# Kernel tuning notes

Measured on AMD Instinct MI355X. Metric: run time of the kernel, lower is better.

## Reference

```python
import jax, jax.numpy as jnp
import numpy as np

N_SENT = 20  # sentence_number


def setup_inputs() -> dict:
    key = jax.random.key(0)
    k1, k2, k3, k4, k5 = jax.random.split(key, 5)
    B, S, D, U = 2048, 800, 100, 50
    inputs = jax.random.normal(k1, (B, S + 1, D), dtype=jnp.float32)
    # keras 'random_normal' initializer default stddev = 0.05
    vw = 0.05 * jax.random.normal(k2, (U, 1), dtype=jnp.float32)
    wh = 0.05 * jax.random.normal(k3, (U, D), dtype=jnp.float32)
    wu = 0.05 * jax.random.normal(k4, (U, D), dtype=jnp.float32)
    bw = 0.05 * jax.random.normal(k5, (U, 1), dtype=jnp.float32)
    return {"inputs": inputs, "vw": vw, "wh": wh, "wu": wu, "bw": bw}


def reference(inputs, vw, wh, wu, bw):
    # inputs: [B, S+1, D]; last row of each item is the user vector
    sent = inputs[:, :-1, :]          # [B, S, D]
    uvec = inputs[:, -1, :]           # [B, D]
    B, S, D = sent.shape
    sec = S // N_SENT
    h = sent.reshape(B, N_SENT, sec, D)               # sections of sentences
    # wu @ user_vec + bw  -> per-batch additive bias  [B, units]
    wub = uvec @ wu.T + bw[:, 0]
    # tanh(h @ wh.T + wub)                              [B, n, s, units]
    t = jnp.tanh(jnp.einsum('bnsd,ud->bnsu', h, wh) + wub[:, None, None, :])
    e = jnp.einsum('bnsu,u->bns', t, vw[:, 0])          # attention logits
    alpha = jax.nn.softmax(e, axis=-1)                  # softmax over section
    out = jnp.einsum('bns,bnsd->bnd', alpha, h)         # weighted pooling
    return out  # [B, N_SENT, D]
```

## Files before the change

### kernel.cpp

```cpp
#include <hip/hip_runtime.h>
#include <hip/hip_bf16.h>
#include <stdint.h>

#define NB    2048
#define NSENT 20
#define SEC   40
#define DD    100
#define UU    50
#define SP1   801
#define STRIDE 136

typedef __attribute__((ext_vector_type(8))) short bf16x8;
typedef __attribute__((ext_vector_type(4))) float f32x4;

__device__ __forceinline__ unsigned f2bf(float f) {
  unsigned u = __float_as_uint(f);
  unsigned r = u + 0x7fffu + ((u >> 16) & 1u);
  return r >> 16;
}

__global__ __launch_bounds__(256, 4) void doc_kernel(
    const float* __restrict__ inputs, const float* __restrict__ vw,
    const float* __restrict__ wh, const float* __restrict__ wu,
    const float* __restrict__ bw, float* __restrict__ out) {
  __shared__ __align__(16) unsigned short hs[2][48 * STRIDE];
  __shared__ __align__(16) float epart[3 * 16 * 4];
  __shared__ float alphas[SEC];
  __shared__ __align__(16) float2 opart[50 * 4];

  const int tid  = threadIdx.x;
  const int w    = tid >> 6, lane = tid & 63;
  const int col  = lane & 15, grp = lane >> 4;
  const int b    = blockIdx.x;

  const float4* base4 = (const float4*)(inputs + (size_t)b * SP1 * DD);

  float4 stage[4];
  #pragma unroll
  for (int j = 0; j < 4; ++j) {
    int idx = j * 256 + tid;
    if (idx < 1000) stage[j] = base4[idx];
  }

  {
    uint4 z; z.x = z.y = z.z = z.w = 0u;
    uint4* p = (uint4*)&hs[0][0];
    #pragma unroll 1
    for (int i = tid; i < 2 * 48 * STRIDE / 8; i += 256) p[i] = z;
  }

  bf16x8 afrag[4];
  {
    int u = w * 16 + col;
    #pragma unroll
    for (int kt = 0; kt < 4; ++kt) {
      bf16x8 f;
      #pragma unroll
      for (int j = 0; j < 8; ++j) {
        int k = kt * 32 + grp * 8 + j;
        float v = (u < UU && k < DD) ? wh[u * DD + k] : 0.f;
        f[j] = (short)f2bf(v);
      }
      afrag[kt] = f;
    }
  }

  float wubacc;
  {
    int ur = lane < UU ? lane : UU - 1;
    const float4* uv4 = (const float4*)(inputs + ((size_t)b * SP1 + SP1 - 1) * DD);
    const float4* wr4 = (const float4*)(wu + ur * DD);
    float a0 = bw[ur];
    #pragma unroll 5
    for (int q = 0; q < 25; ++q) {
      float4 uq = uv4[q], wq = wr4[q];
      a0 = fmaf(uq.x, wq.x, a0); a0 = fmaf(uq.y, wq.y, a0);
      a0 = fmaf(uq.z, wq.z, a0); a0 = fmaf(uq.w, wq.w, a0);
    }
    wubacc = a0;
  }
  float vwr[4], wubr[4];
  #pragma unroll
  for (int r = 0; r < 4; ++r) {
    int u = w * 16 + grp * 4 + r;
    float wv = __shfl(wubacc, u & 63);
    bool val = (u < UU);
    vwr[r]  = val ? vw[u] : 0.f;
    wubr[r] = val ? wv : 0.f;
  }

  __syncthreads();

  float* outb = out + (size_t)b * NSENT * DD;
  int cur = 0;

  #pragma unroll 1
  for (int t = 0; t < NSENT; ++t) {
    #pragma unroll
    for (int j = 0; j < 4; ++j) {
      int idx = j * 256 + tid;
      if (idx < 1000) {
        int row = idx / 25, c4 = idx - row * 25;
        uint2 wv;
        wv.x = f2bf(stage[j].x) | (f2bf(stage[j].y) << 16);
        wv.y = f2bf(stage[j].z) | (f2bf(stage[j].w) << 16);
        *(uint2*)&hs[cur][row * STRIDE + c4 * 4] = wv;
      }
    }
    __syncthreads();

    if (t + 1 < NSENT) {
      const float4* nb4 = base4 + (size_t)(t + 1) * 1000;
      #pragma unroll
      for (int j = 0; j < 4; ++j) {
        int idx = j * 256 + tid;
        if (idx < 1000) stage[j] = nb4[idx];
      }
    }
    __builtin_amdgcn_sched_barrier(0);

    f32x4 acc[3];
    #pragma unroll
    for (int st = 0; st < 3; ++st) { f32x4 z = {0.f,0.f,0.f,0.f}; acc[st] = z; }
    #pragma unroll
    for (int kt = 0; kt < 4; ++kt) {
      #pragma unroll
      for (int st = 0; st < 3; ++st) {
        bf16x8 hf = *(const bf16x8*)&hs[cur][(st * 16 + col) * STRIDE + kt * 32 + grp * 8];
        acc[st] = __builtin_amdgcn_mfma_f32_16x16x32_bf16(afrag[kt], hf, acc[st], 0, 0, 0);
      }
    }

    #pragma unroll
    for (int st = 0; st < 3; ++st) {
      float s = 0.f;
      #pragma unroll
      for (int r = 0; r < 4; ++r) {
        float x = acc[st][r] + wubr[r];
        x = fminf(fmaxf(x, -15.f), 15.f);
        float E = __expf(2.f * x);
        float tt = 1.f - 2.f * __builtin_amdgcn_rcpf(E + 1.f);
        s = fmaf(tt, vwr[r], s);
      }
      s += __shfl_xor(s, 16);
      s += __shfl_xor(s, 32);
      if (grp == 0) epart[st * 64 + col * 4 + w] = s;
    }
    __syncthreads();

    f32x4 q0 = *(const f32x4*)&epart[0 * 64 + col * 4];
    f32x4 q1 = *(const f32x4*)&epart[1 * 64 + col * 4];
    f32x4 q2 = *(const f32x4*)&epart[2 * 64 + col * 4];
    float e0 = (q0[0] + q0[1]) + (q0[2] + q0[3]);
    float e1 = (q1[0] + q1[1]) + (q1[2] + q1[3]);
    float e2 = (q2[0] + q2[1]) + (q2[2] + q2[3]);
    float mx = fmaxf(e0, e1);
    if (col < 8) mx = fmaxf(mx, e2);
    mx = fmaxf(mx, __shfl_xor(mx, 1));
    mx = fmaxf(mx, __shfl_xor(mx, 2));
    mx = fmaxf(mx, __shfl_xor(mx, 4));
    mx = fmaxf(mx, __shfl_xor(mx, 8));
    float p0 = __expf(e0 - mx);
    float p1 = __expf(e1 - mx);
    float p2 = (col < 8) ? __expf(e2 - mx) : 0.f;
    float sum = p0 + p1 + p2;
    sum += __shfl_xor(sum, 1);
    sum += __shfl_xor(sum, 2);
    sum += __shfl_xor(sum, 4);
    sum += __shfl_xor(sum, 8);
    float rinv = __builtin_amdgcn_rcpf(sum);
    if (w == 0 && grp == 0) {
      alphas[col]      = p0 * rinv;
      alphas[16 + col] = p1 * rinv;
      if (col < 8) alphas[32 + col] = p2 * rinv;
    }
    __syncthreads();

    if (lane < 50) {
      float f0 = 0.f, f1 = 0.f;
      #pragma unroll
      for (int i = 0; i < 10; ++i) {
        int s = w * 10 + i;
        float a = alphas[s];
        unsigned hh = *(const unsigned*)&hs[cur][s * STRIDE + lane * 2];
        f0 = fmaf(a, __uint_as_float(hh << 16), f0);
        f1 = fmaf(a, __uint_as_float(hh & 0xffff0000u), f1);
      }
      float2 o; o.x = f0; o.y = f1;
      opart[lane * 4 + w] = o;
    }
    __syncthreads();

    if (w == 0 && lane < 50) {
      f32x4 a0 = *(const f32x4*)&opart[lane * 4];
      f32x4 a1 = *(const f32x4*)&opart[lane * 4 + 2];
      float2 o;
      o.x = (a0[0] + a0[2]) + (a1[0] + a1[2]);
      o.y = (a0[1] + a0[3]) + (a1[1] + a1[3]);
      *(float2*)(outb + t * DD + lane * 2) = o;
    }
    cur ^= 1;
  }
}

extern "C" void kernel_launch(void* const* d_in, const int* in_sizes, int n_in,
                              void* d_out, int out_size, void* d_ws, size_t ws_size,
                              hipStream_t stream) {
  const float* inputs = (const float*)d_in[0];
  const float* vw     = (const float*)d_in[1];
  const float* wh     = (const float*)d_in[2];
  const float* wu     = (const float*)d_in[3];
  const float* bw     = (const float*)d_in[4];
  float* out = (float*)d_out;

  doc_kernel<<<NB, 256, 0, stream>>>(inputs, vw, wh, wu, bw, out);
}
```

Measured before the change: 165.4 us.

## Stream fp32 sections into LDS via global_load_lds and convert to bf16 at fragment load

Replaces the register staging and bf16 repacking into LDS with direct global-to-LDS asynchronous loads of fp32 section data, double-buffered. The data is converted to bf16 only when building MFMA fragments, and the weighted pooling now reads fp32 directly from LDS with each wave producing 25 output columns, which removes the partial-sum reduction stage. It also drops the tanh input clamp and the softmax max subtraction, which saves instructions but risks overflow for large logits. LDS use roughly doubles per buffer, which may reduce occupancy, and the async prefetch relies on the later barriers for completion.

Result: slower. 184.0 us (+11.3%).

```diff
diff --git a/kernel.cpp b/kernel.cpp
--- a/kernel.cpp
+++ b/kernel.cpp
@@ -8,7 +8,7 @@
 #define DD    100
 #define UU    50
 #define SP1   801
-#define STRIDE 136
+#define FBE   4832
 
 typedef __attribute__((ext_vector_type(8))) short bf16x8;
 typedef __attribute__((ext_vector_type(4))) float f32x4;
@@ -19,34 +19,44 @@
   return r >> 16;
 }
 
+__device__ __forceinline__ bf16x8 cvt8(f32x4 a, f32x4 b) {
+  union { unsigned u[4]; bf16x8 v; } r;
+  asm("v_cvt_pk_bf16_f32 %0, %1, %2" : "=v"(r.u[0]) : "v"(a[0]), "v"(a[1]));
+  asm("v_cvt_pk_bf16_f32 %0, %1, %2" : "=v"(r.u[1]) : "v"(a[2]), "v"(a[3]));
+  asm("v_cvt_pk_bf16_f32 %0, %1, %2" : "=v"(r.u[2]) : "v"(b[0]), "v"(b[1]));
+  asm("v_cvt_pk_bf16_f32 %0, %1, %2" : "=v"(r.u[3]) : "v"(b[2]), "v"(b[3]));
+  return r.v;
+}
+
+#define GL16(gp, lp) __builtin_amdgcn_global_load_lds( \
+    (const __attribute__((address_space(1))) unsigned*)(const void*)(gp), \
+    (__attribute__((address_space(3))) unsigned*)(void*)(lp), 16, 0, 0)
+
 __global__ __launch_bounds__(256, 4) void doc_kernel(
     const float* __restrict__ inputs, const float* __restrict__ vw,
     const float* __restrict__ wh, const float* __restrict__ wu,
     const float* __restrict__ bw, float* __restrict__ out) {
-  __shared__ __align__(16) unsigned short hs[2][48 * STRIDE];
+  __shared__ __align__(16) float fbuf[2][FBE];
   __shared__ __align__(16) float epart[3 * 16 * 4];
   __shared__ float alphas[SEC];
-  __shared__ __align__(16) float2 opart[50 * 4];
 
   const int tid  = threadIdx.x;
   const int w    = tid >> 6, lane = tid & 63;
   const int col  = lane & 15, grp = lane >> 4;
   const int b    = blockIdx.x;
 
-  const float4* base4 = (const float4*)(inputs + (size_t)b * SP1 * DD);
-
-  float4 stage[4];
+  const float* base = inputs + (size_t)b * SP1 * DD;
+
   #pragma unroll
-  for (int j = 0; j < 4; ++j) {
-    int idx = j * 256 + tid;
-    if (idx < 1000) stage[j] = base4[idx];
-  }
-
-  {
-    uint4 z; z.x = z.y = z.z = z.w = 0u;
-    uint4* p = (uint4*)&hs[0][0];
-    #pragma unroll 1
-    for (int i = tid; i < 2 * 48 * STRIDE / 8; i += 256) p[i] = z;
+  for (int c = 0; c < 4; ++c) {
+    int chunk = 4 * w + c;
+    int g = chunk * 64 + lane;
+    if (g < 1000) GL16(base + g * 4, &fbuf[0][chunk * 256]);
+  }
+
+  for (int i = tid; i < 2 * (FBE - 4000); i += 256) {
+    int bb = i >= (FBE - 4000);
+    fbuf[bb][4000 + (i - bb * (FBE - 4000))] = 0.f;
   }
 
   bf16x8 afrag[4];
@@ -96,29 +106,18 @@
 
   #pragma unroll 1
   for (int t = 0; t < NSENT; ++t) {
-    #pragma unroll
-    for (int j = 0; j < 4; ++j) {
-      int idx = j * 256 + tid;
-      if (idx < 1000) {
-        int row = idx / 25, c4 = idx - row * 25;
-        uint2 wv;
-        wv.x = f2bf(stage[j].x) | (f2bf(stage[j].y) << 16);
-        wv.y = f2bf(stage[j].z) | (f2bf(stage[j].w) << 16);
-        *(uint2*)&hs[cur][row * STRIDE + c4 * 4] = wv;
-      }
-    }
-    __syncthreads();
-
     if (t + 1 < NSENT) {
-      const float4* nb4 = base4 + (size_t)(t + 1) * 1000;
-      #pragma unroll
-      for (int j = 0; j < 4; ++j) {
-        int idx = j * 256 + tid;
-        if (idx < 1000) stage[j] = nb4[idx];
-      }
-    }
-    __builtin_amdgcn_sched_barrier(0);
-
+      const float* nb = base + (size_t)(t + 1) * (SEC * DD);
+      float* lb = &fbuf[cur ^ 1][0];
+      #pragma unroll
+      for (int c = 0; c < 4; ++c) {
+        int chunk = 4 * w + c;
+        int g = chunk * 64 + lane;
+        if (g < 1000) GL16(nb + g * 4, lb + chunk * 256);
+      }
+    }
+
+    const float* fb = &fbuf[cur][0];
     f32x4 acc[3];
     #pragma unroll
     for (int st = 0; st < 3; ++st) { f32x4 z = {0.f,0.f,0.f,0.f}; acc[st] = z; }
@@ -126,7 +125,10 @@
     for (int kt = 0; kt < 4; ++kt) {
       #pragma unroll
       for (int st = 0; st < 3; ++st) {
-        bf16x8 hf = *(const bf16x8*)&hs[cur][(st * 16 + col) * STRIDE + kt * 32 + grp * 8];
+        int off = (st * 16 + col) * DD + kt * 32 + grp * 8;
+        f32x4 fa = *(const f32x4*)(fb + off);
+        f32x4 fbv = *(const f32x4*)(fb + off + 4);
+        bf16x8 hf = cvt8(fa, fbv);
         acc[st] = __builtin_amdgcn_mfma_f32_16x16x32_bf16(afrag[kt], hf, acc[st], 0, 0, 0);
       }
     }
@@ -137,7 +139,6 @@
       #pragma unroll
       for (int r = 0; r < 4; ++r) {
         float x = acc[st][r] + wubr[r];
-        x = fminf(fmaxf(x, -15.f), 15.f);
         float E = __expf(2.f * x);
         float tt = 1.f - 2.f * __builtin_amdgcn_rcpf(E + 1.f);
         s = fmaf(tt, vwr[r], s);
@@ -148,21 +149,15 @@
     }
     __syncthreads();
 
-    f32x4 q0 = *(const f32x4*)&epart[0 * 64 + col * 4];
-    f32x4 q1 = *(const f32x4*)&epart[1 * 64 + col * 4];
-    f32x4 q2 = *(const f32x4*)&epart[2 * 64 + col * 4];
+    f32x4 q0 = *(const f32x4*)&epart[col * 4];
+    f32x4 q1 = *(const f32x4*)&epart[64 + col * 4];
+    f32x4 q2 = *(const f32x4*)&epart[128 + col * 4];
     float e0 = (q0[0] + q0[1]) + (q0[2] + q0[3]);
     float e1 = (q1[0] + q1[1]) + (q1[2] + q1[3]);
     float e2 = (q2[0] + q2[1]) + (q2[2] + q2[3]);
-    float mx = fmaxf(e0, e1);
-    if (col < 8) mx = fmaxf(mx, e2);
-    mx = fmaxf(mx, __shfl_xor(mx, 1));
-    mx = fmaxf(mx, __shfl_xor(mx, 2));
-    mx = fmaxf(mx, __shfl_xor(mx, 4));
-    mx = fmaxf(mx, __shfl_xor(mx, 8));
-    float p0 = __expf(e0 - mx);
-    float p1 = __expf(e1 - mx);
-    float p2 = (col < 8) ? __expf(e2 - mx) : 0.f;
+    float p0 = __expf(e0);
+    float p1 = __expf(e1);
+    float p2 = (col < 8) ? __expf(e2) : 0.f;
     float sum = p0 + p1 + p2;
     sum += __shfl_xor(sum, 1);
     sum += __shfl_xor(sum, 2);
@@ -176,29 +171,17 @@
     }
     __syncthreads();
 
-    if (lane < 50) {
-      float f0 = 0.f, f1 = 0.f;
-      #pragma unroll
-      for (int i = 0; i < 10; ++i) {
-        int s = w * 10 + i;
-        float a = alphas[s];
-        unsigned hh = *(const unsigned*)&hs[cur][s * STRIDE + lane * 2];
-        f0 = fmaf(a, __uint_as_float(hh << 16), f0);
-        f1 = fmaf(a, __uint_as_float(hh & 0xffff0000u), f1);
-      }
-      float2 o; o.x = f0; o.y = f1;
-      opart[lane * 4 + w] = o;
+    if (lane < 25) {
+      const float* colp = fb + 25 * w + lane;
+      float a0 = 0.f, a1 = 0.f;
+      #pragma unroll
+      for (int s = 0; s < SEC; s += 2) {
+        a0 = fmaf(alphas[s],     colp[s * DD], a0);
+        a1 = fmaf(alphas[s + 1], colp[(s + 1) * DD], a1);
+      }
+      outb[t * DD + 25 * w + lane] = a0 + a1;
     }
     __syncthreads();
-
-    if (w == 0 && lane < 50) {
-      f32x4 a0 = *(const f32x4*)&opart[lane * 4];
-      f32x4 a1 = *(const f32x4*)&opart[lane * 4 + 2];
-      float2 o;
-      o.x = (a0[0] + a0[2]) + (a1[0] + a1[2]);
-      o.y = (a0[1] + a0[3]) + (a1[1] + a1[3]);
-      *(float2*)(outb + t * DD + lane * 2) = o;
-    }
     cur ^= 1;
   }
 }
```

## Switch to 32x32x16 MFMA with bias folded into GEMM and swizzled LDS

Applied to the files above, without the earlier changes.

Replaces the 16x16x32 MFMA tiling with 32x32x16 MFMAs split across warps by unit-half and sentence-half. The per-batch bias is folded into the GEMM as an extra K column (a constant 1.0 in the h tile and wub in the weights). The LDS layout is XOR-swizzled to cut bank conflicts, and conversion uses hardware packed bf16 converts. The softmax drops max-subtraction and the alpha LDS round-trip and sync in favour of shuffles. Risks: the bias is now rounded to bf16, and softmax without max subtraction could overflow for large logits.

After: 257.0 us. 55.4% more time.

```diff
diff --git a/kernel.cpp b/kernel.cpp
--- a/kernel.cpp
+++ b/kernel.cpp
@@ -8,30 +8,40 @@
 #define DD    100
 #define UU    50
 #define SP1   801
-#define STRIDE 136
-
-typedef __attribute__((ext_vector_type(8))) short bf16x8;
-typedef __attribute__((ext_vector_type(4))) float f32x4;
+#define ROWB  272
+#define HBUFB (64 * ROWB)
+
+typedef short bf16x8 __attribute__((ext_vector_type(8)));
+typedef short bf16x4 __attribute__((ext_vector_type(4)));
+typedef float f32x16 __attribute__((ext_vector_type(16)));
 
 __device__ __forceinline__ unsigned f2bf(float f) {
   unsigned u = __float_as_uint(f);
-  unsigned r = u + 0x7fffu + ((u >> 16) & 1u);
-  return r >> 16;
-}
+  return (u + 0x7fffu + ((u >> 16) & 1u)) >> 16;
+}
+
+__device__ __forceinline__ void cvt8(float4 a, float4 b, unsigned* o) {
+  asm("v_cvt_pk_bf16_f32 %0, %1, %2" : "=v"(o[0]) : "v"(a.x), "v"(a.y));
+  asm("v_cvt_pk_bf16_f32 %0, %1, %2" : "=v"(o[1]) : "v"(a.z), "v"(a.w));
+  asm("v_cvt_pk_bf16_f32 %0, %1, %2" : "=v"(o[2]) : "v"(b.x), "v"(b.y));
+  asm("v_cvt_pk_bf16_f32 %0, %1, %2" : "=v"(o[3]) : "v"(b.z), "v"(b.w));
+}
+
+#define KEY(row) ((((row) >> 3) & 3) << 3)
 
 __global__ __launch_bounds__(256, 4) void doc_kernel(
     const float* __restrict__ inputs, const float* __restrict__ vw,
     const float* __restrict__ wh, const float* __restrict__ wu,
     const float* __restrict__ bw, float* __restrict__ out) {
-  __shared__ __align__(16) unsigned short hs[2][48 * STRIDE];
-  __shared__ __align__(16) float epart[3 * 16 * 4];
-  __shared__ float alphas[SEC];
-  __shared__ __align__(16) float2 opart[50 * 4];
-
-  const int tid  = threadIdx.x;
-  const int w    = tid >> 6, lane = tid & 63;
-  const int col  = lane & 15, grp = lane >> 4;
-  const int b    = blockIdx.x;
+  __shared__ __align__(16) unsigned char hsb[2 * HBUFB];
+  __shared__ __align__(16) float epartf[64 * 2];
+  __shared__ __align__(16) float opartf[50 * 10];
+
+  const int tid = threadIdx.x;
+  const int w = tid >> 6, lane = tid & 63;
+  const int ut = w & 1, st = w >> 1;
+  const int l31 = lane & 31, hh = lane >> 5;
+  const int b = blockIdx.x;
 
   const float4* base4 = (const float4*)(inputs + (size_t)b * SP1 * DD);
 
@@ -44,67 +54,86 @@
 
   {
     uint4 z; z.x = z.y = z.z = z.w = 0u;
-    uint4* p = (uint4*)&hs[0][0];
+    uint4* p = (uint4*)hsb;
     #pragma unroll 1
-    for (int i = tid; i < 2 * 48 * STRIDE / 8; i += 256) p[i] = z;
-  }
-
-  bf16x8 afrag[4];
-  {
-    int u = w * 16 + col;
-    #pragma unroll
-    for (int kt = 0; kt < 4; ++kt) {
-      bf16x8 f;
-      #pragma unroll
-      for (int j = 0; j < 8; ++j) {
-        int k = kt * 32 + grp * 8 + j;
-        float v = (u < UU && k < DD) ? wh[u * DD + k] : 0.f;
-        f[j] = (short)f2bf(v);
-      }
-      afrag[kt] = f;
-    }
-  }
-
-  float wubacc;
-  {
-    int ur = lane < UU ? lane : UU - 1;
+    for (int i = tid; i < 2 * HBUFB / 16; i += 256) p[i] = z;
+  }
+
+  int cvta[4];
+  #pragma unroll
+  for (int j = 0; j < 4; ++j) {
+    int idx = j * 256 + tid;
+    int row = idx / 25, c4 = idx - row * 25;
+    cvta[j] = (row * ROWB + c4 * 8) ^ KEY(row);
+  }
+
+  const int u = l31 + 32 * ut;
+  float wubv = 0.f;
+  if (u < UU) {
     const float4* uv4 = (const float4*)(inputs + ((size_t)b * SP1 + SP1 - 1) * DD);
-    const float4* wr4 = (const float4*)(wu + ur * DD);
-    float a0 = bw[ur];
+    const float4* wr4 = (const float4*)(wu + u * DD);
+    float a0 = bw[u];
     #pragma unroll 5
     for (int q = 0; q < 25; ++q) {
       float4 uq = uv4[q], wq = wr4[q];
       a0 = fmaf(uq.x, wq.x, a0); a0 = fmaf(uq.y, wq.y, a0);
       a0 = fmaf(uq.z, wq.z, a0); a0 = fmaf(uq.w, wq.w, a0);
     }
-    wubacc = a0;
-  }
-  float vwr[4], wubr[4];
-  #pragma unroll
-  for (int r = 0; r < 4; ++r) {
-    int u = w * 16 + grp * 4 + r;
-    float wv = __shfl(wubacc, u & 63);
-    bool val = (u < UU);
-    vwr[r]  = val ? vw[u] : 0.f;
-    wubr[r] = val ? wv : 0.f;
-  }
-
+    wubv = a0;
+  }
+
+  bf16x8 afrag[8];
+  #pragma unroll
+  for (int kt = 0; kt < 8; ++kt) {
+    int k0 = 16 * kt + 8 * hh;
+    float4 fa = {0.f,0.f,0.f,0.f}, fb = {0.f,0.f,0.f,0.f};
+    if (u < UU) {
+      if (k0 + 3 <= 99) fa = *(const float4*)(wh + u * DD + k0);
+      if (k0 + 7 <= 99) fb = *(const float4*)(wh + u * DD + k0 + 4);
+    }
+    union { unsigned uu[4]; bf16x8 v; } r;
+    cvt8(fa, fb, r.uu);
+    if (kt == 6 && hh == 0 && u < UU) {
+      union { unsigned short s[8]; bf16x8 v; } t2; t2.v = r.v;
+      t2.s[4] = (unsigned short)f2bf(wubv);
+      r.v = t2.v;
+    }
+    afrag[kt] = r.v;
+  }
+
+  float vwr[16];
+  #pragma unroll
+  for (int i = 0; i < 16; ++i) {
+    int row = (i & 3) + 8 * (i >> 2) + 4 * hh;
+    int ui = 32 * ut + row;
+    vwr[i] = (ui < UU) ? vw[ui] : 0.f;
+  }
+
+  if (tid < 80) {
+    int buf = tid / SEC, s = tid - buf * SEC;
+    int byte = buf * HBUFB + ((s * ROWB + 200) ^ KEY(s));
+    *(unsigned short*)(hsb + byte) = 0x3F80;
+  }
   __syncthreads();
 
+  const int brow = l31 + 32 * st;
+  const int brb = brow * ROWB, bkey = KEY(brow);
+
   float* outb = out + (size_t)b * NSENT * DD;
-  int cur = 0;
 
   #pragma unroll 1
   for (int t = 0; t < NSENT; ++t) {
+    unsigned char* hcur = hsb + (t & 1) * HBUFB;
+
     #pragma unroll
     for (int j = 0; j < 4; ++j) {
       int idx = j * 256 + tid;
       if (idx < 1000) {
-        int row = idx / 25, c4 = idx - row * 25;
-        uint2 wv;
-        wv.x = f2bf(stage[j].x) | (f2bf(stage[j].y) << 16);
-        wv.y = f2bf(stage[j].z) | (f2bf(stage[j].w) << 16);
-        *(uint2*)&hs[cur][row * STRIDE + c4 * 4] = wv;
+        unsigned o[4];
+        cvt8(make_float4(stage[j].x, stage[j].y, stage[j].z, stage[j].w),
+             make_float4(0.f,0.f,0.f,0.f), o);
+        uint2 wv; wv.x = o[0]; wv.y = o[1];
+        *(uint2*)(hcur + cvta[j]) = wv;
       }
     }
     __syncthreads();
@@ -119,87 +148,62 @@
     }
     __builtin_amdgcn_sched_barrier(0);
 
-    f32x4 acc[3];
+    f32x16 acc = {0.f,0.f,0.f,0.f,0.f,0.f,0.f,0.f,0.f,0.f,0.f,0.f,0.f,0.f,0.f,0.f};
     #pragma unroll
-    for (int st = 0; st < 3; ++st) { f32x4 z = {0.f,0.f,0.f,0.f}; acc[st] = z; }
+    for (int kt = 0; kt < 8; ++kt) {
+      int x = 32 * kt + 16 * hh;
+      bf16x4 lo = *(const bf16x4*)(hcur + ((brb + x) ^ bkey));
+      bf16x4 hi = *(const bf16x4*)(hcur + ((brb + x + 8) ^ bkey));
+      bf16x8 bf = __builtin_shufflevector(lo, hi, 0,1,2,3,4,5,6,7);
+      acc = __builtin_amdgcn_mfma_f32_32x32x16_bf16(afrag[kt], bf, acc, 0, 0, 0);
+    }
+
+    float ep = 0.f;
     #pragma unroll
-    for (int kt = 0; kt < 4; ++kt) {
-      #pragma unroll
-      for (int st = 0; st < 3; ++st) {
-        bf16x8 hf = *(const bf16x8*)&hs[cur][(st * 16 + col) * STRIDE + kt * 32 + grp * 8];
-        acc[st] = __builtin_amdgcn_mfma_f32_16x16x32_bf16(afrag[kt], hf, acc[st], 0, 0, 0);
-      }
-    }
-
-    #pragma unroll
-    for (int st = 0; st < 3; ++st) {
-      float s = 0.f;
-      #pragma unroll
-      for (int r = 0; r < 4; ++r) {
-        float x = acc[st][r] + wubr[r];
-        x = fminf(fmaxf(x, -15.f), 15.f);
-        float E = __expf(2.f * x);
-        float tt = 1.f - 2.f * __builtin_amdgcn_rcpf(E + 1.f);
-        s = fmaf(tt, vwr[r], s);
-      }
-      s += __shfl_xor(s, 16);
-      s += __shfl_xor(s, 32);
-      if (grp == 0) epart[st * 64 + col * 4 + w] = s;
-    }
+    for (int i = 0; i < 16; ++i) {
+      float E = exp2f(acc[i] * 2.885390081777927f);
+      float tt = 1.f - 2.f * __builtin_amdgcn_rcpf(E + 1.f);
+      ep = fmaf(tt, vwr[i], ep);
+    }
+    ep += __shfl_xor(ep, 32);
+    if (lane < 32)
+      epartf[(32 * st + l31) * 2 + ut] = ep;
     __syncthreads();
 
-    f32x4 q0 = *(const f32x4*)&epart[0 * 64 + col * 4];
-    f32x4 q1 = *(const f32x4*)&epart[1 * 64 + col * 4];
-    f32x4 q2 = *(const f32x4*)&epart[2 * 64 + col * 4];
-    float e0 = (q0[0] + q0[1]) + (q0[2] + q0[3]);
-    float e1 = (q1[0] + q1[1]) + (q1[2] + q1[3]);
-    float e2 = (q2[0] + q2[1]) + (q2[2] + q2[3]);
-    float mx = fmaxf(e0, e1);
-    if (col < 8) mx = fmaxf(mx, e2);
-    mx = fmaxf(mx, __shfl_xor(mx, 1));
-    mx = fmaxf(mx, __shfl_xor(mx, 2));
-    mx = fmaxf(mx, __shfl_xor(mx, 4));
-    mx = fmaxf(mx, __shfl_xor(mx, 8));
-    float p0 = __expf(e0 - mx);
-    float p1 = __expf(e1 - mx);
-    float p2 = (col < 8) ? __expf(e2 - mx) : 0.f;
-    float sum = p0 + p1 + p2;
+    float2 e2 = (lane < SEC) ? *(const float2*)&epartf[2 * lane]
+                             : make_float2(0.f, 0.f);
+    float p = (lane < SEC) ? __expf(e2.x + e2.y) : 0.f;
+    float sum = p;
     sum += __shfl_xor(sum, 1);
     sum += __shfl_xor(sum, 2);
     sum += __shfl_xor(sum, 4);
     sum += __shfl_xor(sum, 8);
-    float rinv = __builtin_amdgcn_rcpf(sum);
-    if (w == 0 && grp == 0) {
-      alphas[col]      = p0 * rinv;
-      alphas[16 + col] = p1 * rinv;
-      if (col < 8) alphas[32 + col] = p2 * rinv;
-    }
-    __syncthreads();
+    sum += __shfl_xor(sum, 16);
+    sum += __shfl_xor(sum, 32);
+    float pr = p * __builtin_amdgcn_rcpf(sum);
 
     if (lane < 50) {
       float f0 = 0.f, f1 = 0.f;
       #pragma unroll
       for (int i = 0; i < 10; ++i) {
-        int s = w * 10 + i;
-        float a = alphas[s];
-        unsigned hh = *(const unsigned*)&hs[cur][s * STRIDE + lane * 2];
-        f0 = fmaf(a, __uint_as_float(hh << 16), f0);
-        f1 = fmaf(a, __uint_as_float(hh & 0xffff0000u), f1);
+        int s = 10 * w + i;
+        float a = __shfl(pr, s);
+        unsigned hv = *(const unsigned*)(hcur + ((s * ROWB + 4 * lane) ^ KEY(s)));
+        f0 = fmaf(a, __uint_as_float(hv << 16), f0);
+        f1 = fmaf(a, __uint_as_float(hv & 0xffff0000u), f1);
       }
-      float2 o; o.x = f0; o.y = f1;
-      opart[lane * 4 + w] = o;
+      *(float2*)&opartf[lane * 10 + w * 2] = make_float2(f0, f1);
     }
     __syncthreads();
 
     if (w == 0 && lane < 50) {
-      f32x4 a0 = *(const f32x4*)&opart[lane * 4];
-      f32x4 a1 = *(const f32x4*)&opart[lane * 4 + 2];
+      const float2* op = (const float2*)&opartf[lane * 10];
+      float2 o0 = op[0], o1 = op[1], o2 = op[2], o3 = op[3];
       float2 o;
-      o.x = (a0[0] + a0[2]) + (a1[0] + a1[2]);
-      o.y = (a0[1] + a0[3]) + (a1[1] + a1[3]);
-      *(float2*)(outb + t * DD + lane * 2) = o;
-    }
-    cur ^= 1;
+      o.x = (o0.x + o1.x) + (o2.x + o3.x);
+      o.y = (o0.y + o1.y) + (o2.y + o3.y);
+      *(float2*)(outb + t * DD + 2 * lane) = o;
+    }
   }
 }
 
```

## Compute softmax per wave and pool over all sentences to drop block barriers

Applied to the files above, without the earlier changes.

Every wave now computes the 40-way softmax redundantly in its own lanes. It broadcasts the alpha weights with readlane, and each wave pools 25 output dims across all sentences, writing straight to global memory. This removes the alphas and opart shared buffers and two __syncthreads per iteration. It also drops the max-subtraction in the softmax and the tanh input clamp, which is safe only while the logits stay bounded by the vw magnitudes. Smaller changes: bf16 conversion uses the v_cvt_pk_bf16_f32 instruction, store offsets are precomputed, and the launch-bounds occupancy hint rises from 4 to 5.

Result: slower. 171.8 us (+3.9%).

```diff
diff --git a/kernel.cpp b/kernel.cpp
--- a/kernel.cpp
+++ b/kernel.cpp
@@ -10,23 +10,20 @@
 #define SP1   801
 #define STRIDE 136
 
-typedef __attribute__((ext_vector_type(8))) short bf16x8;
-typedef __attribute__((ext_vector_type(4))) float f32x4;
+typedef short bf16x8 __attribute__((ext_vector_type(8)));
+typedef float f32x4 __attribute__((ext_vector_type(4)));
 
 __device__ __forceinline__ unsigned f2bf(float f) {
   unsigned u = __float_as_uint(f);
-  unsigned r = u + 0x7fffu + ((u >> 16) & 1u);
-  return r >> 16;
+  return (u + 0x7fffu + ((u >> 16) & 1u)) >> 16;
 }
 
-__global__ __launch_bounds__(256, 4) void doc_kernel(
+__global__ __launch_bounds__(256, 5) void doc_kernel(
     const float* __restrict__ inputs, const float* __restrict__ vw,
     const float* __restrict__ wh, const float* __restrict__ wu,
     const float* __restrict__ bw, float* __restrict__ out) {
   __shared__ __align__(16) unsigned short hs[2][48 * STRIDE];
   __shared__ __align__(16) float epart[3 * 16 * 4];
-  __shared__ float alphas[SEC];
-  __shared__ __align__(16) float2 opart[50 * 4];
 
   const int tid  = threadIdx.x;
   const int w    = tid >> 6, lane = tid & 63;
@@ -47,6 +44,14 @@
     uint4* p = (uint4*)&hs[0][0];
     #pragma unroll 1
     for (int i = tid; i < 2 * 48 * STRIDE / 8; i += 256) p[i] = z;
+  }
+
+  int cvta[4];
+  #pragma unroll
+  for (int j = 0; j < 4; ++j) {
+    int idx = j * 256 + tid;
+    int row = idx / 25, c4 = idx - row * 25;
+    cvta[j] = row * 272 + c4 * 8;
   }
 
   bf16x8 afrag[4];
@@ -92,19 +97,20 @@
   __syncthreads();
 
   float* outb = out + (size_t)b * NSENT * DD;
-  int cur = 0;
 
   #pragma unroll 1
   for (int t = 0; t < NSENT; ++t) {
+    unsigned char* hc = (unsigned char*)&hs[t & 1][0];
+
     #pragma unroll
     for (int j = 0; j < 4; ++j) {
       int idx = j * 256 + tid;
       if (idx < 1000) {
-        int row = idx / 25, c4 = idx - row * 25;
-        uint2 wv;
-        wv.x = f2bf(stage[j].x) | (f2bf(stage[j].y) << 16);
-        wv.y = f2bf(stage[j].z) | (f2bf(stage[j].w) << 16);
-        *(uint2*)&hs[cur][row * STRIDE + c4 * 4] = wv;
+        unsigned o0, o1;
+        asm("v_cvt_pk_bf16_f32 %0, %1, %2" : "=v"(o0) : "v"(stage[j].x), "v"(stage[j].y));
+        asm("v_cvt_pk_bf16_f32 %0, %1, %2" : "=v"(o1) : "v"(stage[j].z), "v"(stage[j].w));
+        uint2 wv; wv.x = o0; wv.y = o1;
+        *(uint2*)(hc + cvta[j]) = wv;
       }
     }
     __syncthreads();
@@ -126,7 +132,7 @@
     for (int kt = 0; kt < 4; ++kt) {
       #pragma unroll
       for (int st = 0; st < 3; ++st) {
-        bf16x8 hf = *(const bf16x8*)&hs[cur][(st * 16 + col) * STRIDE + kt * 32 + grp * 8];
+        bf16x8 hf = *(const bf16x8*)(hc + (st * 16 + col) * 272 + kt * 64 + grp * 16);
         acc[st] = __builtin_amdgcn_mfma_f32_16x16x32_bf16(afrag[kt], hf, acc[st], 0, 0, 0);
       }
     }
@@ -137,7 +143,6 @@
       #pragma unroll
       for (int r = 0; r < 4; ++r) {
         float x = acc[st][r] + wubr[r];
-        x = fminf(fmaxf(x, -15.f), 15.f);
         float E = __expf(2.f * x);
         float tt = 1.f - 2.f * __builtin_amdgcn_rcpf(E + 1.f);
         s = fmaf(tt, vwr[r], s);
@@ -148,58 +153,33 @@
     }
     __syncthreads();
 
-    f32x4 q0 = *(const f32x4*)&epart[0 * 64 + col * 4];
-    f32x4 q1 = *(const f32x4*)&epart[1 * 64 + col * 4];
-    f32x4 q2 = *(const f32x4*)&epart[2 * 64 + col * 4];
-    float e0 = (q0[0] + q0[1]) + (q0[2] + q0[3]);
-    float e1 = (q1[0] + q1[1]) + (q1[2] + q1[3]);
-    float e2 = (q2[0] + q2[1]) + (q2[2] + q2[3]);
-    float mx = fmaxf(e0, e1);
-    if (col < 8) mx = fmaxf(mx, e2);
-    mx = fmaxf(mx, __shfl_xor(mx, 1));
-    mx = fmaxf(mx, __shfl_xor(mx, 2));
-    mx = fmaxf(mx, __shfl_xor(mx, 4));
-    mx = fmaxf(mx, __shfl_xor(mx, 8));
-    float p0 = __expf(e0 - mx);
-    float p1 = __expf(e1 - mx);
-    float p2 = (col < 8) ? __expf(e2 - mx) : 0.f;
-    float sum = p0 + p1 + p2;
+    int sl = lane < SEC ? lane : 0;
+    f32x4 q = *(const f32x4*)&epart[(sl >> 4) * 64 + (sl & 15) * 4];
+    float e = (q[0] + q[1]) + (q[2] + q[3]);
+    float p = (lane < SEC) ? __expf(e) : 0.f;
+    float sum = p;
     sum += __shfl_xor(sum, 1);
     sum += __shfl_xor(sum, 2);
     sum += __shfl_xor(sum, 4);
     sum += __shfl_xor(sum, 8);
-    float rinv = __builtin_amdgcn_rcpf(sum);
-    if (w == 0 && grp == 0) {
-      alphas[col]      = p0 * rinv;
-      alphas[16 + col] = p1 * rinv;
-      if (col < 8) alphas[32 + col] = p2 * rinv;
+    sum += __shfl_xor(sum, 16);
+    sum += __shfl_xor(sum, 32);
+    float pr = p * __builtin_amdgcn_rcpf(sum);
+    asm volatile("" : "+v"(pr));
+
+    if (lane < 25) {
+      int d = 25 * w + lane;
+      const unsigned short* hp = (const unsigned short*)hc + d;
+      float a0 = 0.f, a1 = 0.f;
+      #pragma unroll
+      for (int s = 0; s < SEC; s += 2) {
+        float al0 = __uint_as_float(__builtin_amdgcn_readlane(__float_as_uint(pr), s));
+        float al1 = __uint_as_float(__builtin_amdgcn_readlane(__float_as_uint(pr), s + 1));
+        a0 = fmaf(al0, __uint_as_float((unsigned)hp[s * STRIDE] << 16), a0);
+        a1 = fmaf(al1, __uint_as_float((unsigned)hp[(s + 1) * STRIDE] << 16), a1);
+      }
+      outb[t * DD + d] = a0 + a1;
     }
-    __syncthreads();
-
-    if (lane < 50) {
-      float f0 = 0.f, f1 = 0.f;
-      #pragma unroll
-      for (int i = 0; i < 10; ++i) {
-        int s = w * 10 + i;
-        float a = alphas[s];
-        unsigned hh = *(const unsigned*)&hs[cur][s * STRIDE + lane * 2];
-        f0 = fmaf(a, __uint_as_float(hh << 16), f0);
-        f1 = fmaf(a, __uint_as_float(hh & 0xffff0000u), f1);
-      }
-      float2 o; o.x = f0; o.y = f1;
-      opart[lane * 4 + w] = o;
-    }
-    __syncthreads();
-
-    if (w == 0 && lane < 50) {
-      f32x4 a0 = *(const f32x4*)&opart[lane * 4];
-      f32x4 a1 = *(const f32x4*)&opart[lane * 4 + 2];
-      float2 o;
-      o.x = (a0[0] + a0[2]) + (a1[0] + a1[2]);
-      o.y = (a0[1] + a0[3]) + (a1[1] + a1[3]);
-      *(float2*)(outb + t * DD + lane * 2) = o;
-    }
-    cur ^= 1;
   }
 }
 
```
